# Kernel tuning notes

Hardware: AMD Instinct MI355X
Metric: run time of the kernel (lower is better)

The kernel has to match this reference:

```python
import jax, jax.numpy as jnp
import numpy as np


def _reduce1(x):
    # x: [B, n, d] -> [B, 2d]; exists=max, forall=min over objects (exclude_self is a no-op for cnt=1)
    return jnp.concatenate([x.max(axis=1), x.min(axis=1)], axis=-1)


def _reduce2(x):
    # x: [B, n, n, d] -> [B, n, 2d]; exclude_self masks diagonal i==j (0 for exists/max, 1 for forall/min)
    n = x.shape[1]
    diag = jnp.eye(n, dtype=bool)[None, :, :, None]
    exists = jnp.where(diag, 0.0, x).max(axis=2)
    forall = jnp.where(diag, 1.0, x).min(axis=2)
    return jnp.concatenate([exists, forall], axis=-1)


def _layer(f0, f1, f2, p):
    # One LogicLayer step (breadth=2, minmax reducer, exclude_self, sigmoid norm, no hidden layers)
    W0, b0, W1, b1, W2, b2 = p
    B, n, d1 = f1.shape
    # order 0: [self, reduce(order1)]
    g0 = jnp.concatenate([f0, _reduce1(f1)], axis=-1)
    o0 = jax.nn.sigmoid(g0 @ W0 + b0)
    # order 1: [expand(order0), self, reduce(order2)]
    e0 = jnp.broadcast_to(f0[:, None, :], (B, n, f0.shape[-1]))
    g1 = jnp.concatenate([e0, f1, _reduce2(f2)], axis=-1)
    o1 = jax.nn.sigmoid(g1 @ W1 + b1)
    # order 2: [expand(order1), self] then Permutation(2) = cat(x, swap(i,j))
    e1 = jnp.broadcast_to(f1[:, :, None, :], (B, n, n, d1))
    g2 = jnp.concatenate([e1, f2], axis=-1)
    g2 = jnp.concatenate([g2, jnp.swapaxes(g2, 1, 2)], axis=-1)
    o2 = jax.nn.sigmoid(g2 @ W2 + b2)
    return o0, o1, o2


def setup_inputs() -> dict:
    key = jax.random.key(0)
    B, n = 4, 256
    d = [32, 64, 64]
    O = 128
    ks = iter(jax.random.split(key, 64))
    inp = {
        "x0": jax.random.uniform(next(ks), (B, d[0]), dtype=jnp.float32),
        "x1": jax.random.uniform(next(ks), (B, n, d[1]), dtype=jnp.float32),
        "x2": jax.random.uniform(next(ks), (B, n, n, d[2]), dtype=jnp.float32),
    }
    fan_ins = [
        (d[0] + 2 * d[1], d[0] + d[1] + 2 * d[2], 2 * (d[1] + d[2])),  # layer 0
        (O + 2 * O, O + O + 2 * O, 2 * (O + O)),                        # layer 1
        (O + 2 * O, O + O + 2 * O, 2 * (O + O)),                        # layer 2
    ]
    for l, fins in enumerate(fan_ins):
        for o, fin in enumerate(fins):
            inp[f"W{o}_{l}"] = jax.random.normal(next(ks), (fin, O), dtype=jnp.float32) / np.sqrt(fin).astype(np.float32)
            inp[f"b{o}_{l}"] = jnp.zeros((O,), dtype=jnp.float32)
    return inp


def reference(x0, x1, x2,
              W0_0, b0_0, W1_0, b1_0, W2_0, b2_0,
              W0_1, b0_1, W1_1, b1_1, W2_1, b2_1,
              W0_2, b0_2, W1_2, b1_2, W2_2, b2_2):
    f = (x0, x1, x2)
    for p in ((W0_0, b0_0, W1_0, b1_0, W2_0, b2_0),
              (W0_1, b0_1, W1_1, b1_1, W2_1, b2_1),
              (W0_2, b0_2, W1_2, b1_2, W2_2, b2_2)):
        f = _layer(*f, p)
    return f
```

## Files before the change

kernel.cpp:

```cpp
#include <hip/hip_runtime.h>
#include <hip/hip_bf16.h>
#include <cstdint>

#define NN 256
#define NB 4
#define OC 128

using bf16x8_t = __attribute__((ext_vector_type(8))) __bf16;
using f32x4_t  = __attribute__((ext_vector_type(4))) float;

typedef const __attribute__((address_space(1))) uint8_t* gptr1_t;
typedef __attribute__((address_space(3))) uint8_t* lptr3_t;

__device__ __forceinline__ void async_load16(const void* g, void* l) {
  __builtin_amdgcn_global_load_lds((gptr1_t)g, (lptr3_t)l, 16, 0, 0);
}

__device__ __forceinline__ float sigf(float x) {
  return __builtin_amdgcn_rcpf(1.0f + __expf(-x));
}

__device__ __forceinline__ uint16_t f2bf_rne(float f) {
  uint32_t u = __float_as_uint(f);
  uint32_t r = (u + 0x7fffu + ((u >> 16) & 1u)) >> 16;
  return (uint16_t)r;
}

__device__ __forceinline__ void emit_wt(const float* __restrict__ W2,
                                        uint16_t* __restrict__ Wt, int d1,
                                        int d2, int idx) {
  const int K = 2 * d2;
  const int nn = idx / K, k = idx - nn * K;
  const int row = (k < d2) ? (d1 + k) : (2 * d1 + d2 + (k - d2));
  Wt[idx] = f2bf_rne(W2[row * OC + nn]);
}

__device__ __forceinline__ void emit_bt(const float* __restrict__ W1,
                                        const float* __restrict__ W2,
                                        uint16_t* __restrict__ Bt, int D0,
                                        int D1, int D2, int FIN1, int KP,
                                        int idx) {
  const int n = idx / KP, k = idx - n * KP;
  float val = 0.f;
  if (n < 128) {
    if (k < FIN1) val = W1[k * OC + n];
  } else if (n < 256) {
    if (k >= D0 && k < D0 + D1) val = W2[(k - D0) * OC + (n - 128)];
  } else {
    if (k >= D0 && k < D0 + D1) val = W2[(D1 + D2 + (k - D0)) * OC + (n - 256)];
  }
  Bt[idx] = f2bf_rne(val);
}

__global__ __launch_bounds__(256) void prep_reduce(
    const float* __restrict__ W2_0, const float* __restrict__ W2_1,
    const float* __restrict__ W2_2, const float* __restrict__ W1_0,
    const float* __restrict__ W1_1, const float* __restrict__ W1_2,
    const float* __restrict__ x0, const float* __restrict__ x1,
    uint16_t* __restrict__ Wt0, uint16_t* __restrict__ Wt1,
    uint16_t* __restrict__ Wt2, uint16_t* __restrict__ Bt0,
    uint16_t* __restrict__ Bt1, uint16_t* __restrict__ Bt2,
    uint16_t* __restrict__ g1bf0, float* __restrict__ r2b,
    float* __restrict__ r2c, const float* __restrict__ x2,
    uint16_t* __restrict__ x2bf) {
  __shared__ float4 smx[256], smn[256];
  const int blk = blockIdx.x;
  const int tid = threadIdx.x;

  if (blk < 4800) {
    int g = blk * 256 + tid;
    if (g < 16384) { emit_wt(W2_0, Wt0, 64, 64, g); return; }
    g -= 16384;
    if (g < 32768) { emit_wt(W2_1, Wt1, 128, 128, g); return; }
    g -= 32768;
    if (g < 32768) { emit_wt(W2_2, Wt2, 128, 128, g); return; }
    g -= 32768;
    if (g < 98304) { emit_bt(W1_0, W2_0, Bt0, 32, 64, 64, 224, 256, g); return; }
    g -= 98304;
    if (g < 196608) { emit_bt(W1_1, W2_1, Bt1, 128, 128, 128, 512, 512, g); return; }
    g -= 196608;
    if (g < 196608) { emit_bt(W1_2, W2_2, Bt2, 128, 128, 128, 512, 512, g); return; }
    g -= 196608;
    if (g < 131072) {
      const int row = g >> 7, t = g & 127;
      uint16_t* const gp = g1bf0 + (size_t)row * 256;
      if (t < 32) gp[t] = f2bf_rne(x0[(row >> 8) * 32 + t]);
      else if (t < 96) gp[t] = f2bf_rne(x1[(size_t)row * 64 + (t - 32)]);
      else gp[128 + t] = 0;
      return;
    }
    g -= 131072;
    if (g < 262144) { r2b[g] = ((g & 255) < 128) ? 0.f : 1.f; return; }
    g -= 262144;
    if (g < 262144) { r2c[g] = ((g & 255) < 128) ? 0.f : 1.f; }
    return;
  }

  const int bid = blk - 4800;
  const int i = bid & 255;
  const int q = tid & 15, s = tid >> 4;
  const size_t rowbase = ((size_t)bid * NN) * 64 + q * 4;
  float mxA0 = 0.f, mxA1 = 0.f, mxA2 = 0.f, mxA3 = 0.f;
  float mnA0 = 1.f, mnA1 = 1.f, mnA2 = 1.f, mnA3 = 1.f;
  float mxB0 = 0.f, mxB1 = 0.f, mxB2 = 0.f, mxB3 = 0.f;
  float mnB0 = 1.f, mnB1 = 1.f, mnB2 = 1.f, mnB3 = 1.f;
#pragma unroll 2
  for (int t = 0; t < 16; t += 2) {
    const int jA = s + t * 16, jB = jA + 16;
    const float4 xa = *(const float4*)(x2 + rowbase + (size_t)jA * 64);
    const float4 xb = *(const float4*)(x2 + rowbase + (size_t)jB * 64);
    uint2 pa, pb;
    pa.x = (uint32_t)f2bf_rne(xa.x) | ((uint32_t)f2bf_rne(xa.y) << 16);
    pa.y = (uint32_t)f2bf_rne(xa.z) | ((uint32_t)f2bf_rne(xa.w) << 16);
    pb.x = (uint32_t)f2bf_rne(xb.x) | ((uint32_t)f2bf_rne(xb.y) << 16);
    pb.y = (uint32_t)f2bf_rne(xb.z) | ((uint32_t)f2bf_rne(xb.w) << 16);
    *(uint2*)(x2bf + rowbase + (size_t)jA * 64) = pa;
    *(uint2*)(x2bf + rowbase + (size_t)jB * 64) = pb;
    if (jA != i) {
      mxA0 = fmaxf(mxA0, xa.x); mxA1 = fmaxf(mxA1, xa.y);
      mxA2 = fmaxf(mxA2, xa.z); mxA3 = fmaxf(mxA3, xa.w);
      mnA0 = fminf(mnA0, xa.x); mnA1 = fminf(mnA1, xa.y);
      mnA2 = fminf(mnA2, xa.z); mnA3 = fminf(mnA3, xa.w);
    }
    if (jB != i) {
      mxB0 = fmaxf(mxB0, xb.x); mxB1 = fmaxf(mxB1, xb.y);
      mxB2 = fmaxf(mxB2, xb.z); mxB3 = fmaxf(mxB3, xb.w);
      mnB0 = fminf(mnB0, xb.x); mnB1 = fminf(mnB1, xb.y);
      mnB2 = fminf(mnB2, xb.z); mnB3 = fminf(mnB3, xb.w);
    }
  }
  float mx0 = fmaxf(mxA0, mxB0), mx1 = fmaxf(mxA1, mxB1);
  float mx2 = fmaxf(mxA2, mxB2), mx3 = fmaxf(mxA3, mxB3);
  float mn0 = fminf(mnA0, mnB0), mn1 = fminf(mnA1, mnB1);
  float mn2 = fminf(mnA2, mnB2), mn3 = fminf(mnA3, mnB3);
  smx[tid] = make_float4(mx0, mx1, mx2, mx3);
  smn[tid] = make_float4(mn0, mn1, mn2, mn3);
  __syncthreads();
  if (s == 0) {
    for (int ss = 1; ss < 16; ++ss) {
      float4 a = smx[q + ss * 16], c = smn[q + ss * 16];
      mx0 = fmaxf(mx0, a.x); mx1 = fmaxf(mx1, a.y);
      mx2 = fmaxf(mx2, a.z); mx3 = fmaxf(mx3, a.w);
      mn0 = fminf(mn0, c.x); mn1 = fminf(mn1, c.y);
      mn2 = fminf(mn2, c.z); mn3 = fminf(mn3, c.w);
    }
    uint16_t* const g = g1bf0 + (size_t)bid * 256;
    g[96 + q * 4 + 0] = f2bf_rne(mx0); g[96 + q * 4 + 1] = f2bf_rne(mx1);
    g[96 + q * 4 + 2] = f2bf_rne(mx2); g[96 + q * 4 + 3] = f2bf_rne(mx3);
    g[160 + q * 4 + 0] = f2bf_rne(mn0); g[160 + q * 4 + 1] = f2bf_rne(mn1);
    g[160 + q * 4 + 2] = f2bf_rne(mn2); g[160 + q * 4 + 3] = f2bf_rne(mn3);
  }
}

template <int KP, int D0, int D1, bool DUP>
__global__ __launch_bounds__(256) void small_gemm(
    const uint16_t* __restrict__ g1, const uint16_t* __restrict__ Bt,
    const float* __restrict__ b1, const float* __restrict__ b2,
    float* __restrict__ f1out, uint16_t* __restrict__ g1next,
    float* __restrict__ u, float* __restrict__ vT,
    const float* __restrict__ f0in, const float* __restrict__ f1in,
    const float* __restrict__ W0, const float* __restrict__ b0,
    float* __restrict__ f0out) {
  constexpr int NCH = KP / 64;
  const int bid = blockIdx.x;
  const int tid = threadIdx.x;

  __shared__ __align__(16) uint8_t ldsA[8192];
  __shared__ __align__(16) uint8_t ldsB[16384];

  if (bid < 48) {
    const int mt = bid / 3, nt = bid - mt * 3;
    const int m0 = mt * 64, n0 = nt * 128;
    const int wv = tid >> 6, lane = tid & 63;
    const int l15 = lane & 15, l4 = lane >> 4;

    f32x4_t acc[4][2];
#pragma unroll
    for (int a = 0; a < 4; ++a)
#pragma unroll
      for (int q = 0; q < 2; ++q) acc[a][q] = (f32x4_t){0.f, 0.f, 0.f, 0.f};

    for (int c = 0; c < NCH; ++c) {
      const int kbg = c * 64;
#pragma unroll
      for (int t = 0; t < 2; ++t) {
        const int id = wv * 2 + t;
        const int mi = id & 3, ks = id >> 2;
        async_load16(g1 + (size_t)(m0 + mi * 16 + l15) * KP + kbg + ks * 32 + l4 * 8,
                     ldsA + id * 1024);
      }
#pragma unroll
      for (int t = 0; t < 4; ++t) {
        const int id = wv * 4 + t;
        const int ni = id & 7, ks = id >> 3;
        async_load16(Bt + (size_t)(n0 + ni * 16 + l15) * KP + kbg + ks * 32 + l4 * 8,
                     ldsB + id * 1024);
      }
      __syncthreads();
#pragma unroll
      for (int ks = 0; ks < 2; ++ks) {
        bf16x8_t Af[4], Bf[2];
#pragma unroll
        for (int a = 0; a < 4; ++a)
          Af[a] = *(const bf16x8_t*)(ldsA + ((ks * 4 + a) << 10) + (lane << 4));
#pragma unroll
        for (int q = 0; q < 2; ++q)
          Bf[q] = *(const bf16x8_t*)(ldsB + ((ks * 8 + wv * 2 + q) << 10) + (lane << 4));
#pragma unroll
        for (int a = 0; a < 4; ++a)
#pragma unroll
          for (int q = 0; q < 2; ++q)
            acc[a][q] = __builtin_amdgcn_mfma_f32_16x16x32_bf16(Af[a], Bf[q],
                                                                acc[a][q], 0, 0, 0);
      }
      __syncthreads();
    }

    float bias[2];
#pragma unroll
    for (int q = 0; q < 2; ++q) {
      const int cc = wv * 32 + q * 16 + l15;
      bias[q] = (nt == 0) ? b1[cc] : ((nt == 1) ? b2[cc] : 0.f);
    }
#pragma unroll
    for (int a = 0; a < 4; ++a) {
      const int rl = a * 16 + l4 * 4;
#pragma unroll
      for (int r = 0; r < 4; ++r) {
        const size_t bi = m0 + rl + r;
#pragma unroll
        for (int q = 0; q < 2; ++q) {
          const int cc = wv * 32 + q * 16 + l15;
          const float x = acc[a][q][r] + bias[q];
          if (nt == 0) {
            const float val = sigf(x);
            f1out[bi * OC + cc] = val;
            if (DUP) g1next[bi * 512 + 128 + cc] = f2bf_rne(val);
          } else if (nt == 1) {
            u[bi * OC + cc] = x;
          } else {
            const int b = (int)(bi >> 8), j = (int)(bi & 255);
            vT[((size_t)b * OC + cc) * NN + j] = x;
          }
        }
      }
    }
  } else {
    constexpr int FIN0 = D0 + 2 * D1;
    constexpr int S = 256 / D1;
    const int b = bid - 48;
    float* const sm = (float*)ldsA;
    float* const g0 = sm;
    float* const smx = sm + 512;
    float* const smn = sm + 768;
    float* const sval = sm + 1024;
    const int cc = tid & (D1 - 1), ss = tid / D1;
    float mx = -1e30f, mn = 1e30f;
    const float* f1b = f1in + (size_t)b * NN * D1;
    for (int j = ss; j < NN; j += S) {
      const float x = f1b[(size_t)j * D1 + cc];
      mx = fmaxf(mx, x); mn = fminf(mn, x);
    }
    smx[tid] = mx; smn[tid] = mn;
    __syncthreads();
    if (ss == 0) {
      for (int s2 = 1; s2 < S; ++s2) {
        mx = fmaxf(mx, smx[cc + s2 * D1]);
        mn = fminf(mn, smn[cc + s2 * D1]);
      }
      g0[D0 + cc] = mx;
      g0[D0 + D1 + cc] = mn;
    }
    if (tid < D0) g0[tid] = f0in[b * D0 + tid];
    __syncthreads();
    if (tid < OC) {
      float acc = b0[tid];
#pragma unroll 8
      for (int k = 0; k < FIN0; ++k) acc += g0[k] * W0[k * OC + tid];
      const float val = sigf(acc);
      f0out[b * OC + tid] = val;
      sval[tid] = val;
    }
    if (DUP) {
      __syncthreads();
      for (int idx = tid; idx < 256 * 128; idx += 256) {
        const int row = idx >> 7, c2 = idx & 127;
        g1next[((size_t)(b * 256 + row)) * 512 + c2] = f2bf_rne(sval[c2]);
      }
    }
  }
}

__global__ __launch_bounds__(256) void conv_r2_kernel(
    const float* __restrict__ r2, uint16_t* __restrict__ g1next) {
  const int bi = blockIdx.x, t = threadIdx.x;
  g1next[(size_t)bi * 512 + 256 + t] = f2bf_rne(r2[(size_t)bi * 256 + t]);
}

template <int D2, typename OUT_T, bool REDUCE>
__global__ __launch_bounds__(256, 4) void gemm2_kernel(
    const __hip_bfloat16* __restrict__ f2, const uint16_t* __restrict__ Wt,
    const float* __restrict__ u, const float* __restrict__ vT,
    OUT_T* __restrict__ out, float* __restrict__ r2n) {
  constexpr int K = 2 * D2;
  constexpr int NCH = K / 32;
  constexpr bool BF16OUT = (sizeof(OUT_T) == 2);
  constexpr int LDSB = BF16OUT ? (128 * 272) : 32768;
  const int bid = blockIdx.x;
  const int jt = bid & 1, i = (bid >> 1) & 255, b = bid >> 9;
  const int j0 = jt * 128;
  const int tid = threadIdx.x;
  const int wv = tid >> 6, lane = tid & 63;
  const int wr = wv >> 1, wc = wv & 1;
  const int l15 = lane & 15, l4 = lane >> 4;

  __shared__ __align__(16) uint8_t lds[LDSB];
  __shared__ unsigned smax[128], smin[128];

  const __hip_bfloat16* const A1 = f2 + ((size_t)(b * NN + i) * NN + j0) * D2;
  const __hip_bfloat16* const A2 = f2 + ((size_t)(b * NN + j0) * NN + i) * D2;

  f32x4_t acc[4][4];
#pragma unroll
  for (int a = 0; a < 4; ++a)
#pragma unroll
    for (int q = 0; q < 4; ++q) acc[a][q] = (f32x4_t){0.f, 0.f, 0.f, 0.f};

  auto STAGE = [&](int c, int buf) {
    const int kbg = c * 32;
    uint8_t* const bA = lds + buf * 16384;
    uint8_t* const bW = bA + 8192;
    const bool second = (kbg >= D2);
    const __hip_bfloat16* const Ab = second ? A2 : A1;
    const size_t rstride = second ? (size_t)NN * D2 : (size_t)D2;
    const int kbase = second ? (kbg - D2) : kbg;
#pragma unroll
    for (int t = 0; t < 2; ++t) {
      const int mi = wv * 2 + t;
      async_load16(Ab + (size_t)(mi * 16 + l15) * rstride + kbase + l4 * 8,
                   bA + mi * 1024);
    }
#pragma unroll
    for (int t = 0; t < 2; ++t) {
      const int ni = wv * 2 + t;
      async_load16(Wt + (size_t)(ni * 16 + l15) * K + kbg + l4 * 8,
                   bW + ni * 1024);
    }
  };

  auto COMPUTE = [&](int buf) {
    const uint8_t* const bA = lds + buf * 16384;
    const uint8_t* const bW = bA + 8192;
    bf16x8_t Af[4], Bf[4];
#pragma unroll
    for (int a = 0; a < 4; ++a)
      Af[a] = *(const bf16x8_t*)(bA + ((wr * 4 + a) << 10) + (lane << 4));
#pragma unroll
    for (int q = 0; q < 4; ++q)
      Bf[q] = *(const bf16x8_t*)(bW + ((wc * 4 + q) << 10) + (lane << 4));
#pragma unroll
    for (int a = 0; a < 4; ++a)
#pragma unroll
      for (int q = 0; q < 4; ++q)
        acc[a][q] = __builtin_amdgcn_mfma_f32_16x16x32_bf16(Af[a], Bf[q],
                                                            acc[a][q], 0, 0, 0);
  };

  STAGE(0, 0);
#pragma unroll
  for (int c = 0; c < NCH - 1; ++c) {
    STAGE(c + 1, (c + 1) & 1);
    asm volatile("s_waitcnt vmcnt(4)" ::: "memory");
    __builtin_amdgcn_sched_barrier(0);
    __builtin_amdgcn_s_barrier();
    __builtin_amdgcn_sched_barrier(0);
    COMPUTE(c & 1);
    asm volatile("s_waitcnt lgkmcnt(0)" ::: "memory");
    __builtin_amdgcn_sched_barrier(0);
    __builtin_amdgcn_s_barrier();
    __builtin_amdgcn_sched_barrier(0);
  }
  asm volatile("s_waitcnt vmcnt(0)" ::: "memory");
  __builtin_amdgcn_sched_barrier(0);
  __builtin_amdgcn_s_barrier();
  __builtin_amdgcn_sched_barrier(0);
  COMPUTE((NCH - 1) & 1);
  __syncthreads();

  const size_t bi2 = (size_t)(b * NN + i);
  float uval[4];
#pragma unroll
  for (int q = 0; q < 4; ++q) uval[q] = u[bi2 * OC + wc * 64 + q * 16 + l15];
  const size_t obase = (bi2 * NN + j0) * OC;
  const float* const vTb = vT + (size_t)b * OC * NN;

  if (BF16OUT) {
    if (REDUCE && tid < 128) { smax[tid] = 0u; smin[tid] = 0x3f800000u; }
    __syncthreads();
    float lmx[4] = {0.f, 0.f, 0.f, 0.f};
    float lmn[4] = {1.f, 1.f, 1.f, 1.f};
#pragma unroll
    for (int a = 0; a < 4; ++a) {
      const int rowb = wr * 64 + a * 16 + l4 * 4;
      const int jg = j0 + rowb;
#pragma unroll
      for (int q = 0; q < 4; ++q) {
        const int col = wc * 64 + q * 16 + l15;
        const float4 vq = *(const float4*)(vTb + (size_t)col * NN + jg);
#pragma unroll
        for (int r = 0; r < 4; ++r) {
          const int j = rowb + r;
          const float x = acc[a][q][r] + uval[q] + ((const float*)&vq)[r];
          const float sg = sigf(x);
          *(uint16_t*)(lds + j * 272 + col * 2) = f2bf_rne(sg);
          if (REDUCE && (jg + r) != i) {
            lmx[q] = fmaxf(lmx[q], sg);
            lmn[q] = fminf(lmn[q], sg);
          }
        }
      }
    }
    if (REDUCE) {
#pragma unroll
      for (int q = 0; q < 4; ++q) {
        const int col = wc * 64 + q * 16 + l15;
        atomicMax(&smax[col], __float_as_uint(lmx[q]));
        atomicMin(&smin[col], __float_as_uint(lmn[q]));
      }
    }
    __syncthreads();
    uint16_t* const outp = (uint16_t*)out;
#pragma unroll
    for (int ci = 0; ci < 8; ++ci) {
      const int chunk = ci * 256 + tid;
      const int row = chunk >> 4, off = chunk & 15;
      const uint4 val = *(const uint4*)(lds + row * 272 + off * 16);
      *(uint4*)(outp + obase + (size_t)row * OC + off * 8) = val;
    }
    if (REDUCE && tid < 128) {
      unsigned* const r2u = (unsigned*)r2n;
      atomicMax(&r2u[bi2 * 256 + tid], smax[tid]);
      atomicMin(&r2u[bi2 * 256 + 128 + tid], smin[tid]);
    }
  } else {
    float* const outp = (float*)out;
#pragma unroll
    for (int a = 0; a < 4; ++a) {
      const int rowb = wr * 64 + a * 16 + l4 * 4;
      const int jg = j0 + rowb;
#pragma unroll
      for (int q = 0; q < 4; ++q) {
        const int col = wc * 64 + q * 16 + l15;
        const float4 vq = *(const float4*)(vTb + (size_t)col * NN + jg);
#pragma unroll
        for (int r = 0; r < 4; ++r) {
          const int j = rowb + r;
          const float x = acc[a][q][r] + uval[q] + ((const float*)&vq)[r];
          outp[obase + (size_t)j * OC + col] = sigf(x);
        }
      }
    }
  }
}

extern "C" void kernel_launch(void* const* d_in, const int* in_sizes, int n_in,
                              void* d_out, int out_size, void* d_ws,
                              size_t ws_size, hipStream_t stream) {
  const float* x0 = (const float*)d_in[0];
  const float* x1 = (const float*)d_in[1];
  const float* x2 = (const float*)d_in[2];
  const float *Wp[3][3], *bp[3][3];
  for (int l = 0; l < 3; ++l)
    for (int o = 0; o < 3; ++o) {
      Wp[l][o] = (const float*)d_in[3 + l * 6 + o * 2];
      bp[l][o] = (const float*)d_in[3 + l * 6 + o * 2 + 1];
    }

  const size_t F2E = (size_t)NB * NN * NN * OC;
  const size_t X2E = (size_t)NB * NN * NN * 64;

  uint8_t* ws = (uint8_t*)d_ws;
  size_t off = 0;
  auto carve = [&](size_t bytes) -> uint8_t* {
    uint8_t* p = ws + off;
    off += (bytes + 255) & ~(size_t)255;
    return p;
  };
  float* f0a = (float*)carve((size_t)NB * OC * 4);
  float* f0b = (float*)carve((size_t)NB * OC * 4);
  float* f1a = (float*)carve((size_t)NB * NN * OC * 4);
  float* f1b = (float*)carve((size_t)NB * NN * OC * 4);
  float* r2b = (float*)carve((size_t)NB * NN * 256 * 4);
  float* r2c = (float*)carve((size_t)NB * NN * 256 * 4);
  float* uu  = (float*)carve((size_t)NB * NN * OC * 4);
  float* vT  = (float*)carve((size_t)NB * OC * NN * 4);
  uint16_t* Wt0 = (uint16_t*)carve((size_t)OC * 128 * 2);
  uint16_t* Wt1 = (uint16_t*)carve((size_t)OC * 256 * 2);
  uint16_t* Wt2 = (uint16_t*)carve((size_t)OC * 256 * 2);
  uint16_t* Bt0 = (uint16_t*)carve((size_t)384 * 256 * 2);
  uint16_t* Bt1 = (uint16_t*)carve((size_t)384 * 512 * 2);
  uint16_t* Bt2 = (uint16_t*)carve((size_t)384 * 512 * 2);
  uint16_t* g1bf0 = (uint16_t*)carve((size_t)NB * NN * 256 * 2);
  uint16_t* g1bf1 = (uint16_t*)carve((size_t)NB * NN * 512 * 2);
  uint16_t* g1bf2 = (uint16_t*)carve((size_t)NB * NN * 512 * 2);
  __hip_bfloat16* f2a = (__hip_bfloat16*)carve(F2E * 2);

  __hip_bfloat16* f2b;
  uint16_t* x2bf;
  if (ws_size >= off + F2E * 2) {
    f2b = (__hip_bfloat16*)carve(F2E * 2);
    x2bf = (uint16_t*)f2b;
  } else {
    f2b = (__hip_bfloat16*)d_in[2];
    x2bf = (uint16_t*)carve(X2E * 2);
  }

  float* out_f0 = (float*)d_out;
  float* out_f1 = out_f0 + (size_t)NB * OC;
  float* out_f2 = out_f1 + (size_t)NB * NN * OC;

  prep_reduce<<<4800 + NB * NN, 256, 0, stream>>>(
      Wp[0][2], Wp[1][2], Wp[2][2], Wp[0][1], Wp[1][1], Wp[2][1], x0, x1, Wt0,
      Wt1, Wt2, Bt0, Bt1, Bt2, g1bf0, r2b, r2c, x2, x2bf);

  small_gemm<256, 32, 64, true><<<52, 256, 0, stream>>>(
      g1bf0, Bt0, bp[0][1], bp[0][2], f1a, g1bf1, uu, vT, x0, x1, Wp[0][0],
      bp[0][0], f0a);
  gemm2_kernel<64, __hip_bfloat16, true><<<NB * NN * 2, 256, 0, stream>>>(
      (const __hip_bfloat16*)x2bf, Wt0, uu, vT, f2a, r2b);
  conv_r2_kernel<<<NB * NN, 256, 0, stream>>>(r2b, g1bf1);

  small_gemm<512, 128, 128, true><<<52, 256, 0, stream>>>(
      g1bf1, Bt1, bp[1][1], bp[1][2], f1b, g1bf2, uu, vT, f0a, f1a, Wp[1][0],
      bp[1][0], f0b);
  gemm2_kernel<128, __hip_bfloat16, true><<<NB * NN * 2, 256, 0, stream>>>(
      f2a, Wt1, uu, vT, f2b, r2c);
  conv_r2_kernel<<<NB * NN, 256, 0, stream>>>(r2c, g1bf2);

  small_gemm<512, 128, 128, false><<<52, 256, 0, stream>>>(
      g1bf2, Bt2, bp[2][1], bp[2][2], out_f1, nullptr, uu, vT, f0b, f1b,
      Wp[2][0], bp[2][0], out_f0);
  gemm2_kernel<128, float, false><<<NB * NN * 2, 256, 0, stream>>>(
      f2b, Wt2, uu, vT, out_f2, nullptr);
}
```

Measured before the change: 514.1 us.

## Rewrite pair GEMM as LDS-free 32x32 MFMA strips with direct global loads

The pair-order GEMM kernel now uses 32-row j-strips per block, eight blocks per (b,i). Each wave computes a 32x32 output tile with 32x32x16 bf16 MFMA, loading A and W fragments straight from global memory instead of double-buffering them through LDS with async loads and barriers. The epilogue writes outputs per lane directly instead of staging through LDS, and occupancy hints are raised. The aim is to remove LDS staging and barrier overhead and to raise parallelism. The cost is redundant weight reads across blocks, strided 2-byte global stores that are poorly coalesced, and reliance on caches to hide latency.

```diff
diff --git a/kernel.cpp b/kernel.cpp
--- a/kernel.cpp
+++ b/kernel.cpp
@@ -8,6 +8,7 @@
 
 using bf16x8_t = __attribute__((ext_vector_type(8))) __bf16;
 using f32x4_t  = __attribute__((ext_vector_type(4))) float;
+using f32x16_t = __attribute__((ext_vector_type(16))) float;
 
 typedef const __attribute__((address_space(1))) uint8_t* gptr1_t;
 typedef __attribute__((address_space(3))) uint8_t* lptr3_t;
@@ -298,166 +299,97 @@
 }
 
 template <int D2, typename OUT_T, bool REDUCE>
-__global__ __launch_bounds__(256, 4) void gemm2_kernel(
+__global__ __launch_bounds__(256, 8) void gemm2_kernel(
     const __hip_bfloat16* __restrict__ f2, const uint16_t* __restrict__ Wt,
     const float* __restrict__ u, const float* __restrict__ vT,
     OUT_T* __restrict__ out, float* __restrict__ r2n) {
   constexpr int K = 2 * D2;
-  constexpr int NCH = K / 32;
+  constexpr int NST = K / 16;
   constexpr bool BF16OUT = (sizeof(OUT_T) == 2);
-  constexpr int LDSB = BF16OUT ? (128 * 272) : 32768;
+
   const int bid = blockIdx.x;
-  const int jt = bid & 1, i = (bid >> 1) & 255, b = bid >> 9;
-  const int j0 = jt * 128;
+  const int strip = bid & 7, i = (bid >> 3) & 255, b = bid >> 11;
+  const int j0 = strip * 32;
   const int tid = threadIdx.x;
   const int wv = tid >> 6, lane = tid & 63;
-  const int wr = wv >> 1, wc = wv & 1;
-  const int l15 = lane & 15, l4 = lane >> 4;
-
-  __shared__ __align__(16) uint8_t lds[LDSB];
+  const int l31 = lane & 31, hi = lane >> 5;
+  const int c0 = wv * 32;
+
   __shared__ unsigned smax[128], smin[128];
 
   const __hip_bfloat16* const A1 = f2 + ((size_t)(b * NN + i) * NN + j0) * D2;
   const __hip_bfloat16* const A2 = f2 + ((size_t)(b * NN + j0) * NN + i) * D2;
-
-  f32x4_t acc[4][4];
-#pragma unroll
-  for (int a = 0; a < 4; ++a)
-#pragma unroll
-    for (int q = 0; q < 4; ++q) acc[a][q] = (f32x4_t){0.f, 0.f, 0.f, 0.f};
-
-  auto STAGE = [&](int c, int buf) {
-    const int kbg = c * 32;
-    uint8_t* const bA = lds + buf * 16384;
-    uint8_t* const bW = bA + 8192;
-    const bool second = (kbg >= D2);
-    const __hip_bfloat16* const Ab = second ? A2 : A1;
-    const size_t rstride = second ? (size_t)NN * D2 : (size_t)D2;
-    const int kbase = second ? (kbg - D2) : kbg;
-#pragma unroll
-    for (int t = 0; t < 2; ++t) {
-      const int mi = wv * 2 + t;
-      async_load16(Ab + (size_t)(mi * 16 + l15) * rstride + kbase + l4 * 8,
-                   bA + mi * 1024);
-    }
-#pragma unroll
-    for (int t = 0; t < 2; ++t) {
-      const int ni = wv * 2 + t;
-      async_load16(Wt + (size_t)(ni * 16 + l15) * K + kbg + l4 * 8,
-                   bW + ni * 1024);
-    }
-  };
-
-  auto COMPUTE = [&](int buf) {
-    const uint8_t* const bA = lds + buf * 16384;
-    const uint8_t* const bW = bA + 8192;
-    bf16x8_t Af[4], Bf[4];
-#pragma unroll
-    for (int a = 0; a < 4; ++a)
-      Af[a] = *(const bf16x8_t*)(bA + ((wr * 4 + a) << 10) + (lane << 4));
-#pragma unroll
-    for (int q = 0; q < 4; ++q)
-      Bf[q] = *(const bf16x8_t*)(bW + ((wc * 4 + q) << 10) + (lane << 4));
-#pragma unroll
-    for (int a = 0; a < 4; ++a)
-#pragma unroll
-      for (int q = 0; q < 4; ++q)
-        acc[a][q] = __builtin_amdgcn_mfma_f32_16x16x32_bf16(Af[a], Bf[q],
-                                                            acc[a][q], 0, 0, 0);
-  };
-
-  STAGE(0, 0);
-#pragma unroll
-  for (int c = 0; c < NCH - 1; ++c) {
-    STAGE(c + 1, (c + 1) & 1);
-    asm volatile("s_waitcnt vmcnt(4)" ::: "memory");
-    __builtin_amdgcn_sched_barrier(0);
-    __builtin_amdgcn_s_barrier();
-    __builtin_amdgcn_sched_barrier(0);
-    COMPUTE(c & 1);
-    asm volatile("s_waitcnt lgkmcnt(0)" ::: "memory");
-    __builtin_amdgcn_sched_barrier(0);
-    __builtin_amdgcn_s_barrier();
-    __builtin_amdgcn_sched_barrier(0);
-  }
-  asm volatile("s_waitcnt vmcnt(0)" ::: "memory");
-  __builtin_amdgcn_sched_barrier(0);
-  __builtin_amdgcn_s_barrier();
-  __builtin_amdgcn_sched_barrier(0);
-  COMPUTE((NCH - 1) & 1);
-  __syncthreads();
+  const __hip_bfloat16* const Wg = (const __hip_bfloat16*)Wt;
+
+  const uint32_t offA1 = (uint32_t)l31 * D2 + hi * 8;
+  const uint32_t offA2 = (uint32_t)l31 * (NN * D2) + hi * 8;
+  const uint32_t offW  = (uint32_t)(c0 + l31) * K + hi * 8;
+
+  f32x16_t acc = {0.f, 0.f, 0.f, 0.f, 0.f, 0.f, 0.f, 0.f,
+                  0.f, 0.f, 0.f, 0.f, 0.f, 0.f, 0.f, 0.f};
+
+#pragma unroll
+  for (int st = 0; st < NST; ++st) {
+    const int kb = st * 16;
+    bf16x8_t Af, Bf;
+    if (kb < D2)
+      Af = *(const bf16x8_t*)(A1 + offA1 + kb);
+    else
+      Af = *(const bf16x8_t*)(A2 + offA2 + (kb - D2));
+    Bf = *(const bf16x8_t*)(Wg + offW + kb);
+    acc = __builtin_amdgcn_mfma_f32_32x32x16_bf16(Af, Bf, acc, 0, 0, 0);
+  }
 
   const size_t bi2 = (size_t)(b * NN + i);
-  float uval[4];
-#pragma unroll
-  for (int q = 0; q < 4; ++q) uval[q] = u[bi2 * OC + wc * 64 + q * 16 + l15];
-  const size_t obase = (bi2 * NN + j0) * OC;
-  const float* const vTb = vT + (size_t)b * OC * NN;
+  const int col = c0 + l31;
+  const float uv = u[bi2 * OC + col];
+  const float* const vTc = vT + ((size_t)b * OC + col) * NN + j0;
+  const size_t obase = (bi2 * NN + j0) * OC + col;
 
   if (BF16OUT) {
-    if (REDUCE && tid < 128) { smax[tid] = 0u; smin[tid] = 0x3f800000u; }
-    __syncthreads();
-    float lmx[4] = {0.f, 0.f, 0.f, 0.f};
-    float lmn[4] = {1.f, 1.f, 1.f, 1.f};
-#pragma unroll
-    for (int a = 0; a < 4; ++a) {
-      const int rowb = wr * 64 + a * 16 + l4 * 4;
-      const int jg = j0 + rowb;
-#pragma unroll
-      for (int q = 0; q < 4; ++q) {
-        const int col = wc * 64 + q * 16 + l15;
-        const float4 vq = *(const float4*)(vTb + (size_t)col * NN + jg);
-#pragma unroll
-        for (int r = 0; r < 4; ++r) {
-          const int j = rowb + r;
-          const float x = acc[a][q][r] + uval[q] + ((const float*)&vq)[r];
-          const float sg = sigf(x);
-          *(uint16_t*)(lds + j * 272 + col * 2) = f2bf_rne(sg);
-          if (REDUCE && (jg + r) != i) {
-            lmx[q] = fmaxf(lmx[q], sg);
-            lmn[q] = fminf(lmn[q], sg);
-          }
+    if (REDUCE) {
+      if (tid < 128) { smax[tid] = 0u; smin[tid] = 0x3f800000u; }
+      __syncthreads();
+    }
+    float lmx = 0.f, lmn = 1.f;
+    uint16_t* const outp = (uint16_t*)out;
+#pragma unroll
+    for (int rg = 0; rg < 4; ++rg) {
+      const int rbase = rg * 8 + 4 * hi;
+      const float4 vq = *(const float4*)(vTc + rbase);
+#pragma unroll
+      for (int rr = 0; rr < 4; ++rr) {
+        const int row = rbase + rr;
+        const float x = acc[rg * 4 + rr] + uv + ((const float*)&vq)[rr];
+        const float sg = sigf(x);
+        outp[obase + (size_t)row * OC] = f2bf_rne(sg);
+        if (REDUCE && (j0 + row) != i) {
+          lmx = fmaxf(lmx, sg);
+          lmn = fminf(lmn, sg);
         }
       }
     }
     if (REDUCE) {
-#pragma unroll
-      for (int q = 0; q < 4; ++q) {
-        const int col = wc * 64 + q * 16 + l15;
-        atomicMax(&smax[col], __float_as_uint(lmx[q]));
-        atomicMin(&smin[col], __float_as_uint(lmn[q]));
-      }
-    }
-    __syncthreads();
-    uint16_t* const outp = (uint16_t*)out;
-#pragma unroll
-    for (int ci = 0; ci < 8; ++ci) {
-      const int chunk = ci * 256 + tid;
-      const int row = chunk >> 4, off = chunk & 15;
-      const uint4 val = *(const uint4*)(lds + row * 272 + off * 16);
-      *(uint4*)(outp + obase + (size_t)row * OC + off * 8) = val;
-    }
-    if (REDUCE && tid < 128) {
-      unsigned* const r2u = (unsigned*)r2n;
-      atomicMax(&r2u[bi2 * 256 + tid], smax[tid]);
-      atomicMin(&r2u[bi2 * 256 + 128 + tid], smin[tid]);
+      atomicMax(&smax[col], __float_as_uint(lmx));
+      atomicMin(&smin[col], __float_as_uint(lmn));
+      __syncthreads();
+      if (tid < 128) {
+        unsigned* const r2u = (unsigned*)r2n;
+        atomicMax(&r2u[bi2 * 256 + tid], smax[tid]);
+        atomicMin(&r2u[bi2 * 256 + 128 + tid], smin[tid]);
+      }
     }
   } else {
     float* const outp = (float*)out;
 #pragma unroll
-    for (int a = 0; a < 4; ++a) {
-      const int rowb = wr * 64 + a * 16 + l4 * 4;
-      const int jg = j0 + rowb;
-#pragma unroll
-      for (int q = 0; q < 4; ++q) {
-        const int col = wc * 64 + q * 16 + l15;
-        const float4 vq = *(const float4*)(vTb + (size_t)col * NN + jg);
-#pragma unroll
-        for (int r = 0; r < 4; ++r) {
-          const int j = rowb + r;
-          const float x = acc[a][q][r] + uval[q] + ((const float*)&vq)[r];
-          outp[obase + (size_t)j * OC + col] = sigf(x);
-        }
+    for (int rg = 0; rg < 4; ++rg) {
+      const int rbase = rg * 8 + 4 * hi;
+      const float4 vq = *(const float4*)(vTc + rbase);
+#pragma unroll
+      for (int rr = 0; rr < 4; ++rr) {
+        const int row = rbase + rr;
+        const float x = acc[rg * 4 + rr] + uv + ((const float*)&vq)[rr];
+        outp[obase + (size_t)row * OC] = sigf(x);
       }
     }
   }
@@ -526,20 +458,20 @@
   small_gemm<256, 32, 64, true><<<52, 256, 0, stream>>>(
       g1bf0, Bt0, bp[0][1], bp[0][2], f1a, g1bf1, uu, vT, x0, x1, Wp[0][0],
       bp[0][0], f0a);
-  gemm2_kernel<64, __hip_bfloat16, true><<<NB * NN * 2, 256, 0, stream>>>(
+  gemm2_kernel<64, __hip_bfloat16, true><<<NB * NN * 8, 256, 0, stream>>>(
       (const __hip_bfloat16*)x2bf, Wt0, uu, vT, f2a, r2b);
   conv_r2_kernel<<<NB * NN, 256, 0, stream>>>(r2b, g1bf1);
 
   small_gemm<512, 128, 128, true><<<52, 256, 0, stream>>>(
       g1bf1, Bt1, bp[1][1], bp[1][2], f1b, g1bf2, uu, vT, f0a, f1a, Wp[1][0],
       bp[1][0], f0b);
-  gemm2_kernel<128, __hip_bfloat16, true><<<NB * NN * 2, 256, 0, stream>>>(
+  gemm2_kernel<128, __hip_bfloat16, true><<<NB * NN * 8, 256, 0, stream>>>(
       f2a, Wt1, uu, vT, f2b, r2c);
   conv_r2_kernel<<<NB * NN, 256, 0, stream>>>(r2c, g1bf2);
 
   small_gemm<512, 128, 128, false><<<52, 256, 0, stream>>>(
       g1bf2, Bt2, bp[2][1], bp[2][2], out_f1, nullptr, uu, vT, f0b, f1b,
       Wp[2][0], bp[2][0], out_f0);
-  gemm2_kernel<128, float, false><<<NB * NN * 2, 256, 0, stream>>>(
+  gemm2_kernel<128, float, false><<<NB * NN * 8, 256, 0, stream>>>(
       f2b, Wt2, uu, vT, out_f2, nullptr);
 }
```

Result: slower. 739.0 us (+43.8%).

## Prefetch all K chunks into LDS upfront and swizzle gemm2 block order

Applied to the files above, without the earlier changes.

Replaces the double-buffered stage/compute loop in gemm2_kernel with one burst that issues async global-to-LDS loads for every K chunk. Each chunk's compute then waits on a decreasing vmcnt and a single barrier, which removes the per-iteration second barrier and keeps many loads in flight. It also remaps block IDs so neighbouring blocks spread across different (b,i) pairs, aimed at better cache behaviour for the transposed A2 reads. The cost is LDS use that grows with K, up to 128KB for the 256-wide layers, which sharply cuts blocks per CU. The launch-bounds occupancy hint is also dropped.

```diff
diff --git a/kernel.cpp b/kernel.cpp
--- a/kernel.cpp
+++ b/kernel.cpp
@@ -14,6 +14,12 @@
 
 __device__ __forceinline__ void async_load16(const void* g, void* l) {
   __builtin_amdgcn_global_load_lds((gptr1_t)g, (lptr3_t)l, 16, 0, 0);
+}
+
+template <int N>
+__device__ __forceinline__ void wvmN() {
+  asm volatile("s_waitcnt vmcnt(%0)" ::"n"(N) : "memory");
+  __builtin_amdgcn_sched_barrier(0);
 }
 
 __device__ __forceinline__ float sigf(float x) {
@@ -298,23 +304,25 @@
 }
 
 template <int D2, typename OUT_T, bool REDUCE>
-__global__ __launch_bounds__(256, 4) void gemm2_kernel(
+__global__ __launch_bounds__(256) void gemm2_kernel(
     const __hip_bfloat16* __restrict__ f2, const uint16_t* __restrict__ Wt,
     const float* __restrict__ u, const float* __restrict__ vT,
     OUT_T* __restrict__ out, float* __restrict__ r2n) {
   constexpr int K = 2 * D2;
   constexpr int NCH = K / 32;
-  constexpr bool BF16OUT = (sizeof(OUT_T) == 2);
-  constexpr int LDSB = BF16OUT ? (128 * 272) : 32768;
+  constexpr int ABYTES = 128 * K * 2;
   const int bid = blockIdx.x;
-  const int jt = bid & 1, i = (bid >> 1) & 255, b = bid >> 9;
+  const int jt = bid & 1;
+  const int pair = bid >> 1;
+  const int sp = (pair & 7) * 128 + (pair >> 3);
+  const int i = sp & 255, b = sp >> 8;
   const int j0 = jt * 128;
   const int tid = threadIdx.x;
   const int wv = tid >> 6, lane = tid & 63;
   const int wr = wv >> 1, wc = wv & 1;
   const int l15 = lane & 15, l4 = lane >> 4;
 
-  __shared__ __align__(16) uint8_t lds[LDSB];
+  __shared__ __align__(16) uint8_t lds[2 * ABYTES];
   __shared__ unsigned smax[128], smin[128];
 
   const __hip_bfloat16* const A1 = f2 + ((size_t)(b * NN + i) * NN + j0) * D2;
@@ -326,31 +334,30 @@
 #pragma unroll
     for (int q = 0; q < 4; ++q) acc[a][q] = (f32x4_t){0.f, 0.f, 0.f, 0.f};
 
-  auto STAGE = [&](int c, int buf) {
+#pragma unroll
+  for (int c = 0; c < NCH; ++c) {
     const int kbg = c * 32;
-    uint8_t* const bA = lds + buf * 16384;
-    uint8_t* const bW = bA + 8192;
     const bool second = (kbg >= D2);
     const __hip_bfloat16* const Ab = second ? A2 : A1;
-    const size_t rstride = second ? (size_t)NN * D2 : (size_t)D2;
+    const size_t rstr = second ? (size_t)NN * D2 : (size_t)D2;
     const int kbase = second ? (kbg - D2) : kbg;
 #pragma unroll
     for (int t = 0; t < 2; ++t) {
       const int mi = wv * 2 + t;
-      async_load16(Ab + (size_t)(mi * 16 + l15) * rstride + kbase + l4 * 8,
-                   bA + mi * 1024);
+      async_load16(Ab + (size_t)(mi * 16 + l15) * rstr + kbase + l4 * 8,
+                   lds + c * 8192 + mi * 1024);
     }
 #pragma unroll
     for (int t = 0; t < 2; ++t) {
       const int ni = wv * 2 + t;
       async_load16(Wt + (size_t)(ni * 16 + l15) * K + kbg + l4 * 8,
-                   bW + ni * 1024);
-    }
-  };
-
-  auto COMPUTE = [&](int buf) {
-    const uint8_t* const bA = lds + buf * 16384;
-    const uint8_t* const bW = bA + 8192;
+                   lds + ABYTES + c * 8192 + ni * 1024);
+    }
+  }
+
+  auto compute_chunk = [&](int c) {
+    const uint8_t* const bA = lds + c * 8192;
+    const uint8_t* const bW = lds + ABYTES + c * 8192;
     bf16x8_t Af[4], Bf[4];
 #pragma unroll
     for (int a = 0; a < 4; ++a)
@@ -366,25 +373,17 @@
                                                             acc[a][q], 0, 0, 0);
   };
 
-  STAGE(0, 0);
-#pragma unroll
-  for (int c = 0; c < NCH - 1; ++c) {
-    STAGE(c + 1, (c + 1) & 1);
-    asm volatile("s_waitcnt vmcnt(4)" ::: "memory");
-    __builtin_amdgcn_sched_barrier(0);
-    __builtin_amdgcn_s_barrier();
-    __builtin_amdgcn_sched_barrier(0);
-    COMPUTE(c & 1);
-    asm volatile("s_waitcnt lgkmcnt(0)" ::: "memory");
-    __builtin_amdgcn_sched_barrier(0);
-    __builtin_amdgcn_s_barrier();
-    __builtin_amdgcn_sched_barrier(0);
-  }
-  asm volatile("s_waitcnt vmcnt(0)" ::: "memory");
-  __builtin_amdgcn_sched_barrier(0);
-  __builtin_amdgcn_s_barrier();
-  __builtin_amdgcn_sched_barrier(0);
-  COMPUTE((NCH - 1) & 1);
+#define G2_STEP(c)                                                     \
+  if constexpr ((c) < NCH) {                                           \
+    wvmN<(NCH - 1 - (c)) * 4>();                                       \
+    __builtin_amdgcn_s_barrier();                                      \
+    __builtin_amdgcn_sched_barrier(0);                                 \
+    compute_chunk(c);                                                  \
+  }
+  G2_STEP(0) G2_STEP(1) G2_STEP(2) G2_STEP(3)
+  G2_STEP(4) G2_STEP(5) G2_STEP(6) G2_STEP(7)
+#undef G2_STEP
+
   __syncthreads();
 
   const size_t bi2 = (size_t)(b * NN + i);
@@ -393,6 +392,7 @@
   for (int q = 0; q < 4; ++q) uval[q] = u[bi2 * OC + wc * 64 + q * 16 + l15];
   const size_t obase = (bi2 * NN + j0) * OC;
   const float* const vTb = vT + (size_t)b * OC * NN;
+  constexpr bool BF16OUT = (sizeof(OUT_T) == 2);
 
   if (BF16OUT) {
     if (REDUCE && tid < 128) { smax[tid] = 0u; smin[tid] = 0x3f800000u; }
```

Measured after the change: 550.2 us. 7.0% more time.
